# Optimization experiments

Measured on AMD Instinct MI355X. Metric: run time of the kernel, lower is better.

Reference implementation:

```python
import jax, jax.numpy as jnp
import numpy as np

V = 32000   # vocab_size
D = 512     # d_model == d_hidden
B = 8       # batch
T = 512     # seq_len
N_LAYERS = 2


def setup_inputs() -> dict:
    key = jax.random.key(0)
    ks = jax.random.split(key, 10)
    tokens = jax.random.randint(ks[0], (B, T), 0, V, dtype=jnp.int32)
    embed = jax.random.normal(ks[1], (V, D), dtype=jnp.float32)  # stddev=1.0 init
    s = 1.0 / np.sqrt(D)
    # per-layer LSTM params: Wx [D,4D], Wh [D,4D], b [4D] (gate order i,f,g,o)
    Wx0 = jax.random.normal(ks[2], (D, 4 * D), dtype=jnp.float32) * s
    Wh0 = jax.random.normal(ks[3], (D, 4 * D), dtype=jnp.float32) * s
    b0 = jnp.zeros((4 * D,), dtype=jnp.float32)
    Wx1 = jax.random.normal(ks[4], (D, 4 * D), dtype=jnp.float32) * s
    Wh1 = jax.random.normal(ks[5], (D, 4 * D), dtype=jnp.float32) * s
    b1 = jnp.zeros((4 * D,), dtype=jnp.float32)
    Wout = jax.random.normal(ks[6], (D, V), dtype=jnp.float32) * s
    bout = jnp.zeros((V,), dtype=jnp.float32)
    return {"tokens": tokens, "embed": embed,
            "Wx0": Wx0, "Wh0": Wh0, "b0": b0,
            "Wx1": Wx1, "Wh1": Wh1, "b1": b1,
            "Wout": Wout, "bout": bout}


def _lstm_layer(x, Wx, Wh, b):
    # x: [B, T, D] -> h_seq: [B, T, D]
    # Precompute input contribution for all timesteps (one big GEMM).
    xW = jnp.einsum('btd,dh->bth', x, Wx) + b  # [B, T, 4D]
    xW_t = jnp.swapaxes(xW, 0, 1)              # [T, B, 4D]
    h0 = jnp.zeros((x.shape[0], Wh.shape[0]), dtype=x.dtype)
    c0 = jnp.zeros_like(h0)

    def step(carry, xw):
        h, c = carry
        gates = xw + h @ Wh                    # [B, 4D]
        i, f, g, o = jnp.split(gates, 4, axis=-1)
        i = jax.nn.sigmoid(i)
        f = jax.nn.sigmoid(f)
        g = jnp.tanh(g)
        o = jax.nn.sigmoid(o)
        c_new = f * c + i * g
        h_new = o * jnp.tanh(c_new)
        return (h_new, c_new), h_new

    _, h_seq = jax.lax.scan(step, (h0, c0), xW_t)  # [T, B, D]
    return jnp.swapaxes(h_seq, 0, 1)


def reference(tokens, embed, Wx0, Wh0, b0, Wx1, Wh1, b1, Wout, bout):
    # ShiftRight(axis=1): prepend zero token, drop last.
    shifted = jnp.pad(tokens, ((0, 0), (1, 0)))[:, :-1]
    x = embed[shifted]                         # [B, T, D]
    x = _lstm_layer(x, Wx0, Wh0, b0)
    x = _lstm_layer(x, Wx1, Wh1, b1)
    # Dropout with deterministic=True is the identity.
    logits = jnp.einsum('btd,dv->btv', x, Wout) + bout  # [B, T, V]
    return logits
```

## Files before the change

### kernel.cpp

```cpp
#include <hip/hip_runtime.h>
#include <cstdint>


typedef float    f32x4  __attribute__((ext_vector_type(4)));
typedef __bf16   bf16x8 __attribute__((ext_vector_type(8)));
typedef uint16_t u16;

constexpr int BB = 8, T = 512, D = 512, V = 32000;
constexpr int M4 = BB * T;
constexpr int G  = 4 * D;
constexpr int FS = 16;

static __device__ __forceinline__ u16 f2bf(float f) {
  union { float f; uint32_t u; } v{f};
  uint32_t r = v.u + 0x7fffu + ((v.u >> 16) & 1u);
  return (u16)(r >> 16);
}
static __device__ __forceinline__ float sigm(float x)  { return 1.f / (1.f + __expf(-x)); }
static __device__ __forceinline__ float tanhr(float x) { return 1.f - 2.f / (__expf(2.f * x) + 1.f); }

__global__ void embed_kernel(const int* __restrict__ tok, const float* __restrict__ emb,
                             u16* __restrict__ Xbf) {
  int m = blockIdx.x;
  int b = m >> 9, t = m & 511;
  int id = t ? tok[b * T + t - 1] : 0;
  const float* src = emb + (size_t)id * D;
  u16* dst = Xbf + (size_t)m * D;
  for (int d = threadIdx.x; d < D; d += 256) dst[d] = f2bf(src[d]);
}

template <bool PERM>
__global__ void transpose_cast(const float* __restrict__ src, u16* __restrict__ dst, int Cn) {
  __shared__ float tl[64][65];
  int n0 = blockIdx.x * 64, k0 = blockIdx.y * 64;
  int tx = threadIdx.x & 63, ty = threadIdx.x >> 6;
  for (int r = ty; r < 64; r += 4) tl[r][tx] = src[(size_t)(k0 + r) * Cn + n0 + tx];
  __syncthreads();
  for (int r = ty; r < 64; r += 4) {
    int n = n0 + r;
    int q = PERM ? ((n & (D - 1)) * 4 + (n >> 9)) : n;
    dst[(size_t)q * D + k0 + tx] = f2bf(tl[tx][r]);
  }
}

__global__ void bias_perm(const float* __restrict__ b, float* __restrict__ bp) {
  int q = blockIdx.x * 256 + threadIdx.x;
  if (q < G) bp[q] = b[(q & 3) * D + (q >> 2)];
}

__global__ __launch_bounds__(256) void gemm_bt(
    const u16* __restrict__ A, const u16* __restrict__ BT,
    const float* __restrict__ bias, float* __restrict__ C, int N, int K) {
  __shared__ u16 As[128 * 32], Bs[128 * 32];
  const int lane = threadIdx.x & 63, wave = threadIdx.x >> 6;
  const int m0 = blockIdx.y * 128, n0 = blockIdx.x * 128;
  const int wm = (wave >> 1) * 64, wn = (wave & 1) * 64;
  const int lr = lane >> 2, lc = (lane & 3) * 8;
  f32x4 acc[4][4] = {};
  for (int kk = 0; kk < K; kk += 32) {
#pragma unroll
    for (int i = 0; i < 2; ++i) {
      int row = wave * 32 + i * 16;
      __builtin_amdgcn_global_load_lds(
          (const __attribute__((address_space(1))) uint32_t*)(A + (size_t)(m0 + row + lr) * K + kk + lc),
          (__attribute__((address_space(3))) uint32_t*)(As + row * 32), 16, 0, 0);
      __builtin_amdgcn_global_load_lds(
          (const __attribute__((address_space(1))) uint32_t*)(BT + (size_t)(n0 + row + lr) * K + kk + lc),
          (__attribute__((address_space(3))) uint32_t*)(Bs + row * 32), 16, 0, 0);
    }
    __syncthreads();
    bf16x8 af[4], bf[4];
#pragma unroll
    for (int i = 0; i < 4; ++i) {
      af[i] = *(const bf16x8*)(As + (wm + i * 16 + (lane & 15)) * 32 + (lane >> 4) * 8);
      bf[i] = *(const bf16x8*)(Bs + (wn + i * 16 + (lane & 15)) * 32 + (lane >> 4) * 8);
    }
#pragma unroll
    for (int mi = 0; mi < 4; ++mi)
#pragma unroll
      for (int ni = 0; ni < 4; ++ni)
        acc[mi][ni] = __builtin_amdgcn_mfma_f32_16x16x32_bf16(af[mi], bf[ni], acc[mi][ni], 0, 0, 0);
    __syncthreads();
  }
  const int cr = (lane >> 4) * 4, cc = lane & 15;
#pragma unroll
  for (int ni = 0; ni < 4; ++ni) {
    int col = n0 + wn + ni * 16 + cc;
    float bv = bias[col];
#pragma unroll
    for (int mi = 0; mi < 4; ++mi) {
      size_t base = (size_t)(m0 + wm + mi * 16 + cr) * N + col;
#pragma unroll
      for (int r = 0; r < 4; ++r) C[base + (size_t)r * N] = acc[mi][ni][r] + bv;
    }
  }
}

__global__ __launch_bounds__(256, 1) void lstm_fused(
    const u16* __restrict__ WhT0, const u16* __restrict__ WhT1, const u16* __restrict__ WxT1,
    const float* __restrict__ xw0, const float* __restrict__ b1p,
    u16* __restrict__ H0ring, u16* __restrict__ H1ring, u16* __restrict__ Hseq1,
    int* __restrict__ flags) {
  __shared__ float Cst[4][16][16];
  const int tid = threadIdx.x, lane = tid & 63, wave = tid >> 6, wg = blockIdx.x;
  const bool L1 = wg >= 32;
  const int wgl = L1 ? wg - 32 : wg;
  const int q16 = wgl * 64 + wave * 16;
  const int fr = lane & 15, quad = lane >> 4;
  const bool gl = lane < 32;
  const int b = lane & 7, dl = (lane >> 3) & 3;
  const int dbase = wgl * 16 + wave * 4;

  if (!L1) {
    bf16x8 whf[16];
#pragma unroll
    for (int kb = 0; kb < 16; ++kb)
      whf[kb] = *(const bf16x8*)(WhT0 + (size_t)(q16 + fr) * 512 + kb * 32 + quad * 8);
    float c_state = 0.f;
    for (int t = 0; t < T; ++t) {
      const int thr = t - ((lane >= 32) ? 1 : 0);
      for (;;) {
        int v = __hip_atomic_load(&flags[lane * FS], __ATOMIC_ACQUIRE, __HIP_MEMORY_SCOPE_AGENT);
        if (__all(v >= thr)) break;
        __builtin_amdgcn_s_sleep(1);
      }
      float4 x4 = *(const float4*)(xw0 + (size_t)(b * T + t) * G + q16 + dl * 4);
      const u16* hA = H0ring + ((t & 1) ^ 1) * 8192;
      f32x4 acc0 = {}, acc1 = {};
#pragma unroll
      for (int kb = 0; kb < 16; kb += 2) {
        bf16x8 a0 = *(const bf16x8*)(hA + fr * 512 + kb * 32 + quad * 8);
        acc0 = __builtin_amdgcn_mfma_f32_16x16x32_bf16(a0, whf[kb], acc0, 0, 0, 0);
        bf16x8 a1 = *(const bf16x8*)(hA + fr * 512 + (kb + 1) * 32 + quad * 8);
        acc1 = __builtin_amdgcn_mfma_f32_16x16x32_bf16(a1, whf[kb + 1], acc1, 0, 0, 0);
      }
      f32x4 acc = acc0 + acc1;
#pragma unroll
      for (int r = 0; r < 4; ++r) Cst[wave][quad * 4 + r][fr] = acc[r];
      int hv = 0;
      if (gl) {
        float pi = Cst[wave][b][dl * 4 + 0] + x4.x;
        float pf = Cst[wave][b][dl * 4 + 1] + x4.y;
        float pg = Cst[wave][b][dl * 4 + 2] + x4.z;
        float po = Cst[wave][b][dl * 4 + 3] + x4.w;
        float ig = sigm(pi), fg = sigm(pf), gg = tanhr(pg), og = sigm(po);
        c_state = fg * c_state + ig * gg;
        hv = f2bf(og * tanhr(c_state));
        int g0 = __shfl(hv, b + 0), g1 = __shfl(hv, b + 8);
        int g2 = __shfl(hv, b + 16), g3 = __shfl(hv, b + 24);
        if (lane < 8) {
          ushort4 p = { (u16)g0, (u16)g1, (u16)g2, (u16)g3 };
          *(ushort4*)(H0ring + (t & 1) * 8192 + b * 512 + dbase) = p;
        }
      }
      __syncthreads();
      if (tid == 0)
        __hip_atomic_store(&flags[wg * FS], t + 1, __ATOMIC_RELEASE, __HIP_MEMORY_SCOPE_AGENT);
    }
  } else {
    bf16x8 whf[16], wxf[16];
#pragma unroll
    for (int kb = 0; kb < 16; ++kb) {
      whf[kb] = *(const bf16x8*)(WhT1 + (size_t)(q16 + fr) * 512 + kb * 32 + quad * 8);
      wxf[kb] = *(const bf16x8*)(WxT1 + (size_t)(q16 + fr) * 512 + kb * 32 + quad * 8);
    }
    float4 bias4 = *(const float4*)(b1p + q16 + dl * 4);
    float c_state = 0.f;
    for (int t = 0; t < T; ++t) {
      const int thr = t + 1 - ((lane >= 32) ? 1 : 0);
      for (;;) {
        int v = __hip_atomic_load(&flags[lane * FS], __ATOMIC_ACQUIRE, __HIP_MEMORY_SCOPE_AGENT);
        if (__all(v >= thr)) break;
        __builtin_amdgcn_s_sleep(1);
      }
      const u16* hA0 = H0ring + (t & 1) * 8192;
      const u16* hA1 = H1ring + ((t & 1) ^ 1) * 8192;
      f32x4 acc0 = {}, acc1 = {}, acc2 = {}, acc3 = {};
#pragma unroll
      for (int kb = 0; kb < 16; kb += 2) {
        bf16x8 a0 = *(const bf16x8*)(hA0 + fr * 512 + kb * 32 + quad * 8);
        acc0 = __builtin_amdgcn_mfma_f32_16x16x32_bf16(a0, wxf[kb], acc0, 0, 0, 0);
        bf16x8 a1 = *(const bf16x8*)(hA1 + fr * 512 + kb * 32 + quad * 8);
        acc1 = __builtin_amdgcn_mfma_f32_16x16x32_bf16(a1, whf[kb], acc1, 0, 0, 0);
        bf16x8 a2 = *(const bf16x8*)(hA0 + fr * 512 + (kb + 1) * 32 + quad * 8);
        acc2 = __builtin_amdgcn_mfma_f32_16x16x32_bf16(a2, wxf[kb + 1], acc2, 0, 0, 0);
        bf16x8 a3 = *(const bf16x8*)(hA1 + fr * 512 + (kb + 1) * 32 + quad * 8);
        acc3 = __builtin_amdgcn_mfma_f32_16x16x32_bf16(a3, whf[kb + 1], acc3, 0, 0, 0);
      }
      f32x4 acc = (acc0 + acc1) + (acc2 + acc3);
#pragma unroll
      for (int r = 0; r < 4; ++r) Cst[wave][quad * 4 + r][fr] = acc[r];
      int hv = 0; ushort4 p;
      if (gl) {
        float pi = Cst[wave][b][dl * 4 + 0] + bias4.x;
        float pf = Cst[wave][b][dl * 4 + 1] + bias4.y;
        float pg = Cst[wave][b][dl * 4 + 2] + bias4.z;
        float po = Cst[wave][b][dl * 4 + 3] + bias4.w;
        float ig = sigm(pi), fg = sigm(pf), gg = tanhr(pg), og = sigm(po);
        c_state = fg * c_state + ig * gg;
        hv = f2bf(og * tanhr(c_state));
        int g0 = __shfl(hv, b + 0), g1 = __shfl(hv, b + 8);
        int g2 = __shfl(hv, b + 16), g3 = __shfl(hv, b + 24);
        p = { (u16)g0, (u16)g1, (u16)g2, (u16)g3 };
        if (lane < 8)
          *(ushort4*)(H1ring + (t & 1) * 8192 + b * 512 + dbase) = p;
      }
      __syncthreads();
      if (tid == 0)
        __hip_atomic_store(&flags[wg * FS], t + 1, __ATOMIC_RELEASE, __HIP_MEMORY_SCOPE_AGENT);
      if (gl && lane < 8)
        *(ushort4*)(Hseq1 + (size_t)(b * T + t) * 512 + dbase) = p;
    }
  }
}

extern "C" void kernel_launch(void* const* d_in, const int* in_sizes, int n_in,
                              void* d_out, int out_size, void* d_ws, size_t ws_size,
                              hipStream_t stream) {
  (void)in_sizes; (void)n_in; (void)out_size; (void)ws_size;
  const int*   tokens = (const int*)d_in[0];
  const float* embed  = (const float*)d_in[1];
  const float* Wx0 = (const float*)d_in[2];
  const float* Wh0 = (const float*)d_in[3];
  const float* b0  = (const float*)d_in[4];
  const float* Wx1 = (const float*)d_in[5];
  const float* Wh1 = (const float*)d_in[6];
  const float* b1  = (const float*)d_in[7];
  const float* Wout = (const float*)d_in[8];
  const float* bout = (const float*)d_in[9];

  char* ws = (char*)d_ws;
  size_t off = 0;
  auto alloc = [&](size_t bytes) -> char* {
    char* p = ws + off; off += (bytes + 255) & ~(size_t)255; return p;
  };
  float* xw  = (float*)alloc((size_t)M4 * G * 4);
  u16* WoutT = (u16*)xw;
  u16* Xbf   = (u16*)alloc((size_t)M4 * D * 2);
  u16* WxT0  = (u16*)alloc((size_t)G * D * 2);
  u16* WhT0  = (u16*)alloc((size_t)G * D * 2);
  u16* WxT1  = (u16*)alloc((size_t)G * D * 2);
  u16* WhT1  = (u16*)alloc((size_t)G * D * 2);
  u16* Hseq1 = (u16*)alloc((size_t)M4 * D * 2);
  float* b0p = (float*)alloc(G * 4);
  float* b1p = (float*)alloc(G * 4);
  char* zbase = ws + off;
  u16* H0ring = (u16*)alloc(2 * 16 * 512 * 2);
  u16* H1ring = (u16*)alloc(2 * 16 * 512 * 2);
  int* flags  = (int*)alloc(64 * FS * 4);
  size_t zbytes = (size_t)((ws + off) - zbase);
  hipMemsetAsync(zbase, 0, zbytes, stream);

  embed_kernel<<<M4, 256, 0, stream>>>(tokens, embed, Xbf);
  transpose_cast<true ><<<dim3(G / 64, 8), 256, 0, stream>>>(Wx0, WxT0, G);
  transpose_cast<true ><<<dim3(G / 64, 8), 256, 0, stream>>>(Wh0, WhT0, G);
  transpose_cast<true ><<<dim3(G / 64, 8), 256, 0, stream>>>(Wx1, WxT1, G);
  transpose_cast<true ><<<dim3(G / 64, 8), 256, 0, stream>>>(Wh1, WhT1, G);
  bias_perm<<<G / 256, 256, 0, stream>>>(b0, b0p);
  bias_perm<<<G / 256, 256, 0, stream>>>(b1, b1p);

  gemm_bt<<<dim3(G / 128, M4 / 128), 256, 0, stream>>>(Xbf, WxT0, b0p, xw, G, D);
  lstm_fused<<<64, 256, 0, stream>>>(WhT0, WhT1, WxT1, xw, b1p, H0ring, H1ring, Hseq1, flags);
  transpose_cast<false><<<dim3(V / 64, 8), 256, 0, stream>>>(Wout, WoutT, V);
  gemm_bt<<<dim3(V / 128, M4 / 128), 256, 0, stream>>>(Hseq1, WoutT, bout, (float*)d_out, V, D);
}
```

Before: 5.619 ms.

## Co-locate both LSTM layers per workgroup in a wavefront-skewed single loop

The persistent LSTM kernel previously used 64 workgroups, 32 per layer, each spinning on flags from all 64 peers every step. Now 32 workgroups each own the same gate columns for both layers and run a skewed loop: at step f they compute layer 0 at time f and layer 1 at time f-1, sharing the loaded h0 fragments between Wh0 and Wx1. This halves the number of flags polled and removes one layer of cross-workgroup dependency per step. In exchange each wave holds three weight fragment sets in registers and does more serial MFMA work per step.

```diff
diff --git a/kernel.cpp b/kernel.cpp
--- a/kernel.cpp
+++ b/kernel.cpp
@@ -103,114 +103,100 @@
     int* __restrict__ flags) {
   __shared__ float Cst[4][16][16];
   const int tid = threadIdx.x, lane = tid & 63, wave = tid >> 6, wg = blockIdx.x;
-  const bool L1 = wg >= 32;
-  const int wgl = L1 ? wg - 32 : wg;
-  const int q16 = wgl * 64 + wave * 16;
+  const int wvg = wg * 4 + wave;
+  const int q16 = wvg * 16;
   const int fr = lane & 15, quad = lane >> 4;
   const bool gl = lane < 32;
   const int b = lane & 7, dl = (lane >> 3) & 3;
-  const int dbase = wgl * 16 + wave * 4;
-
-  if (!L1) {
-    bf16x8 whf[16];
-#pragma unroll
-    for (int kb = 0; kb < 16; ++kb)
-      whf[kb] = *(const bf16x8*)(WhT0 + (size_t)(q16 + fr) * 512 + kb * 32 + quad * 8);
-    float c_state = 0.f;
-    for (int t = 0; t < T; ++t) {
-      const int thr = t - ((lane >= 32) ? 1 : 0);
-      for (;;) {
-        int v = __hip_atomic_load(&flags[lane * FS], __ATOMIC_ACQUIRE, __HIP_MEMORY_SCOPE_AGENT);
-        if (__all(v >= thr)) break;
-        __builtin_amdgcn_s_sleep(1);
-      }
-      float4 x4 = *(const float4*)(xw0 + (size_t)(b * T + t) * G + q16 + dl * 4);
-      const u16* hA = H0ring + ((t & 1) ^ 1) * 8192;
-      f32x4 acc0 = {}, acc1 = {};
-#pragma unroll
-      for (int kb = 0; kb < 16; kb += 2) {
-        bf16x8 a0 = *(const bf16x8*)(hA + fr * 512 + kb * 32 + quad * 8);
-        acc0 = __builtin_amdgcn_mfma_f32_16x16x32_bf16(a0, whf[kb], acc0, 0, 0, 0);
-        bf16x8 a1 = *(const bf16x8*)(hA + fr * 512 + (kb + 1) * 32 + quad * 8);
-        acc1 = __builtin_amdgcn_mfma_f32_16x16x32_bf16(a1, whf[kb + 1], acc1, 0, 0, 0);
-      }
-      f32x4 acc = acc0 + acc1;
+  const int dbase = wvg * 4;
+
+  bf16x8 whf0[16], whf1[16], wxf1[16];
+#pragma unroll
+  for (int kb = 0; kb < 16; ++kb) {
+    whf0[kb] = *(const bf16x8*)(WhT0 + (size_t)(q16 + fr) * 512 + kb * 32 + quad * 8);
+    whf1[kb] = *(const bf16x8*)(WhT1 + (size_t)(q16 + fr) * 512 + kb * 32 + quad * 8);
+    wxf1[kb] = *(const bf16x8*)(WxT1 + (size_t)(q16 + fr) * 512 + kb * 32 + quad * 8);
+  }
+  float4 bias4 = *(const float4*)(b1p + q16 + dl * 4);
+
+  float c0 = 0.f, c1 = 0.f;
+  for (int f = 0; f <= T; ++f) {
+    const bool doL0 = (f < T), doL1 = (f >= 1);
+    float4 x4;
+    if (doL0 && gl) x4 = *(const float4*)(xw0 + (size_t)(b * T + f) * G + q16 + dl * 4);
+    for (;;) {
+      int v = f;
+      if (lane < 32) v = __hip_atomic_load(&flags[lane * FS], __ATOMIC_ACQUIRE, __HIP_MEMORY_SCOPE_AGENT);
+      if (__all(v >= f)) break;
+      __builtin_amdgcn_s_sleep(1);
+    }
+    const u16* h0p = H0ring + ((f & 1) ^ 1) * 8192;
+    const u16* h1p = H1ring + (f & 1) * 8192;
+    f32x4 acA0 = {}, acA1 = {}, acB0 = {}, acB1 = {};
+#pragma unroll
+    for (int kb = 0; kb < 16; kb += 2) {
+      bf16x8 a0 = *(const bf16x8*)(h0p + fr * 512 + kb * 32 + quad * 8);
+      bf16x8 a1 = *(const bf16x8*)(h0p + fr * 512 + (kb + 1) * 32 + quad * 8);
+      if (doL0) {
+        acA0 = __builtin_amdgcn_mfma_f32_16x16x32_bf16(a0, whf0[kb], acA0, 0, 0, 0);
+        acA1 = __builtin_amdgcn_mfma_f32_16x16x32_bf16(a1, whf0[kb + 1], acA1, 0, 0, 0);
+      }
+      if (doL1) {
+        acB0 = __builtin_amdgcn_mfma_f32_16x16x32_bf16(a0, wxf1[kb], acB0, 0, 0, 0);
+        acB1 = __builtin_amdgcn_mfma_f32_16x16x32_bf16(a1, wxf1[kb + 1], acB1, 0, 0, 0);
+        bf16x8 b0v = *(const bf16x8*)(h1p + fr * 512 + kb * 32 + quad * 8);
+        bf16x8 b1v = *(const bf16x8*)(h1p + fr * 512 + (kb + 1) * 32 + quad * 8);
+        acB0 = __builtin_amdgcn_mfma_f32_16x16x32_bf16(b0v, whf1[kb], acB0, 0, 0, 0);
+        acB1 = __builtin_amdgcn_mfma_f32_16x16x32_bf16(b1v, whf1[kb + 1], acB1, 0, 0, 0);
+      }
+    }
+    if (doL0) {
+      f32x4 acc = acA0 + acA1;
 #pragma unroll
       for (int r = 0; r < 4; ++r) Cst[wave][quad * 4 + r][fr] = acc[r];
-      int hv = 0;
       if (gl) {
         float pi = Cst[wave][b][dl * 4 + 0] + x4.x;
         float pf = Cst[wave][b][dl * 4 + 1] + x4.y;
         float pg = Cst[wave][b][dl * 4 + 2] + x4.z;
         float po = Cst[wave][b][dl * 4 + 3] + x4.w;
         float ig = sigm(pi), fg = sigm(pf), gg = tanhr(pg), og = sigm(po);
-        c_state = fg * c_state + ig * gg;
-        hv = f2bf(og * tanhr(c_state));
+        c0 = fg * c0 + ig * gg;
+        int hv = f2bf(og * tanhr(c0));
         int g0 = __shfl(hv, b + 0), g1 = __shfl(hv, b + 8);
         int g2 = __shfl(hv, b + 16), g3 = __shfl(hv, b + 24);
         if (lane < 8) {
-          ushort4 p = { (u16)g0, (u16)g1, (u16)g2, (u16)g3 };
-          *(ushort4*)(H0ring + (t & 1) * 8192 + b * 512 + dbase) = p;
+          ushort4 pk = { (u16)g0, (u16)g1, (u16)g2, (u16)g3 };
+          *(ushort4*)(H0ring + (f & 1) * 8192 + b * 512 + dbase) = pk;
         }
       }
-      __syncthreads();
-      if (tid == 0)
-        __hip_atomic_store(&flags[wg * FS], t + 1, __ATOMIC_RELEASE, __HIP_MEMORY_SCOPE_AGENT);
-    }
-  } else {
-    bf16x8 whf[16], wxf[16];
-#pragma unroll
-    for (int kb = 0; kb < 16; ++kb) {
-      whf[kb] = *(const bf16x8*)(WhT1 + (size_t)(q16 + fr) * 512 + kb * 32 + quad * 8);
-      wxf[kb] = *(const bf16x8*)(WxT1 + (size_t)(q16 + fr) * 512 + kb * 32 + quad * 8);
-    }
-    float4 bias4 = *(const float4*)(b1p + q16 + dl * 4);
-    float c_state = 0.f;
-    for (int t = 0; t < T; ++t) {
-      const int thr = t + 1 - ((lane >= 32) ? 1 : 0);
-      for (;;) {
-        int v = __hip_atomic_load(&flags[lane * FS], __ATOMIC_ACQUIRE, __HIP_MEMORY_SCOPE_AGENT);
-        if (__all(v >= thr)) break;
-        __builtin_amdgcn_s_sleep(1);
-      }
-      const u16* hA0 = H0ring + (t & 1) * 8192;
-      const u16* hA1 = H1ring + ((t & 1) ^ 1) * 8192;
-      f32x4 acc0 = {}, acc1 = {}, acc2 = {}, acc3 = {};
-#pragma unroll
-      for (int kb = 0; kb < 16; kb += 2) {
-        bf16x8 a0 = *(const bf16x8*)(hA0 + fr * 512 + kb * 32 + quad * 8);
-        acc0 = __builtin_amdgcn_mfma_f32_16x16x32_bf16(a0, wxf[kb], acc0, 0, 0, 0);
-        bf16x8 a1 = *(const bf16x8*)(hA1 + fr * 512 + kb * 32 + quad * 8);
-        acc1 = __builtin_amdgcn_mfma_f32_16x16x32_bf16(a1, whf[kb], acc1, 0, 0, 0);
-        bf16x8 a2 = *(const bf16x8*)(hA0 + fr * 512 + (kb + 1) * 32 + quad * 8);
-        acc2 = __builtin_amdgcn_mfma_f32_16x16x32_bf16(a2, wxf[kb + 1], acc2, 0, 0, 0);
-        bf16x8 a3 = *(const bf16x8*)(hA1 + fr * 512 + (kb + 1) * 32 + quad * 8);
-        acc3 = __builtin_amdgcn_mfma_f32_16x16x32_bf16(a3, whf[kb + 1], acc3, 0, 0, 0);
-      }
-      f32x4 acc = (acc0 + acc1) + (acc2 + acc3);
+    }
+    ushort4 p; bool st1 = false;
+    if (doL1) {
+      f32x4 acc = acB0 + acB1;
 #pragma unroll
       for (int r = 0; r < 4; ++r) Cst[wave][quad * 4 + r][fr] = acc[r];
-      int hv = 0; ushort4 p;
       if (gl) {
         float pi = Cst[wave][b][dl * 4 + 0] + bias4.x;
         float pf = Cst[wave][b][dl * 4 + 1] + bias4.y;
         float pg = Cst[wave][b][dl * 4 + 2] + bias4.z;
         float po = Cst[wave][b][dl * 4 + 3] + bias4.w;
         float ig = sigm(pi), fg = sigm(pf), gg = tanhr(pg), og = sigm(po);
-        c_state = fg * c_state + ig * gg;
-        hv = f2bf(og * tanhr(c_state));
+        c1 = fg * c1 + ig * gg;
+        int hv = f2bf(og * tanhr(c1));
         int g0 = __shfl(hv, b + 0), g1 = __shfl(hv, b + 8);
         int g2 = __shfl(hv, b + 16), g3 = __shfl(hv, b + 24);
         p = { (u16)g0, (u16)g1, (u16)g2, (u16)g3 };
-        if (lane < 8)
-          *(ushort4*)(H1ring + (t & 1) * 8192 + b * 512 + dbase) = p;
-      }
-      __syncthreads();
-      if (tid == 0)
-        __hip_atomic_store(&flags[wg * FS], t + 1, __ATOMIC_RELEASE, __HIP_MEMORY_SCOPE_AGENT);
-      if (gl && lane < 8)
-        *(ushort4*)(Hseq1 + (size_t)(b * T + t) * 512 + dbase) = p;
-    }
+        if (lane < 8) {
+          st1 = true;
+          *(ushort4*)(H1ring + ((f - 1) & 1) * 8192 + b * 512 + dbase) = p;
+        }
+      }
+    }
+    __syncthreads();
+    if (tid == 0)
+      __hip_atomic_store(&flags[wg * FS], f + 1, __ATOMIC_RELEASE, __HIP_MEMORY_SCOPE_AGENT);
+    if (st1)
+      *(ushort4*)(Hseq1 + (size_t)(b * T + (f - 1)) * 512 + dbase) = p;
   }
 }
 
@@ -260,7 +246,7 @@
   bias_perm<<<G / 256, 256, 0, stream>>>(b1, b1p);
 
   gemm_bt<<<dim3(G / 128, M4 / 128), 256, 0, stream>>>(Xbf, WxT0, b0p, xw, G, D);
-  lstm_fused<<<64, 256, 0, stream>>>(WhT0, WhT1, WxT1, xw, b1p, H0ring, H1ring, Hseq1, flags);
+  lstm_fused<<<32, 256, 0, stream>>>(WhT0, WhT1, WxT1, xw, b1p, H0ring, H1ring, Hseq1, flags);
   transpose_cast<false><<<dim3(V / 64, 8), 256, 0, stream>>>(Wout, WoutT, V);
   gemm_bt<<<dim3(V / 128, M4 / 128), 256, 0, stream>>>(Hseq1, WoutT, bout, (float*)d_out, V, D);
 }
```

Result: faster. 5.375 ms (-4.3%).
